# Kernel tuning notes

Hardware: AMD Instinct MI355X
Metric: run time of the kernel (lower is better)

The kernel has to match this reference:

```python
import jax, jax.numpy as jnp
import numpy as np

N_NODES = 50000
N_EDGES = 800000
NUM_FEATS = 128
HIDDEN = 256
NUM_GRAPHS = 512
BN_EPS = 1e-5


def setup_inputs() -> dict:
    key = jax.random.key(0)
    ks = jax.random.split(key, 12)
    x = jax.random.normal(ks[0], (N_NODES, NUM_FEATS), dtype=jnp.float32)
    edge_index = jax.random.randint(ks[1], (2, N_EDGES), 0, N_NODES, dtype=jnp.int64)
    batch = jnp.sort(jax.random.randint(ks[2], (N_NODES,), 0, NUM_GRAPHS, dtype=jnp.int64))
    s1 = 1.0 / np.sqrt(NUM_FEATS)
    s2 = 1.0 / np.sqrt(HIDDEN)
    return {
        "x": x,
        "edge_index": edge_index,
        "batch": batch,
        "w1a": jax.random.normal(ks[3], (NUM_FEATS, HIDDEN), dtype=jnp.float32) * s1,
        "b1a": jnp.zeros((HIDDEN,), jnp.float32),
        "w2a": jax.random.normal(ks[4], (HIDDEN, HIDDEN), dtype=jnp.float32) * s2,
        "b2a": jnp.zeros((HIDDEN,), jnp.float32),
        "ga": jnp.ones((HIDDEN,), jnp.float32),
        "ba": jnp.zeros((HIDDEN,), jnp.float32),
        "w1s": jax.random.normal(ks[5], (2, HIDDEN, HIDDEN), dtype=jnp.float32) * s2,
        "b1s": jnp.zeros((2, HIDDEN), jnp.float32),
        "w2s": jax.random.normal(ks[6], (2, HIDDEN, HIDDEN), dtype=jnp.float32) * s2,
        "b2s": jnp.zeros((2, HIDDEN), jnp.float32),
        "gs": jnp.ones((2, HIDDEN), jnp.float32),
        "bs": jnp.zeros((2, HIDDEN), jnp.float32),
    }


def _gin_layer(h, src, dst, w1, b1, w2, b2, gamma, beta):
    # GIN aggregation: (1 + eps=0) * x + sum over in-neighbors
    agg = jax.ops.segment_sum(h[src], dst, num_segments=N_NODES)
    z = h + agg
    z = jax.nn.relu(z @ w1 + b1)
    z = jax.nn.relu(z @ w2 + b2)
    # BatchNorm1d (training mode: biased batch statistics over nodes)
    mu = jnp.mean(z, axis=0)
    var = jnp.var(z, axis=0)
    return gamma * (z - mu) * jax.lax.rsqrt(var + BN_EPS) + beta


def reference(x, edge_index, batch, w1a, b1a, w2a, b2a, ga, ba,
              w1s, b1s, w2s, b2s, gs, bs):
    src, dst = edge_index[0], edge_index[1]
    h = _gin_layer(x, src, dst, w1a, b1a, w2a, b2a, ga, ba)
    for i in range(w1s.shape[0]):
        h = _gin_layer(h, src, dst, w1s[i], b1s[i], w2s[i], b2s[i], gs[i], bs[i])
    # global_mean_pool over graph ids
    sums = jax.ops.segment_sum(h, batch, num_segments=NUM_GRAPHS)
    counts = jax.ops.segment_sum(jnp.ones((h.shape[0],), h.dtype), batch,
                                 num_segments=NUM_GRAPHS)
    return sums / jnp.maximum(counts, 1.0)[:, None]
```

## Files before the change

kernel.cpp:

```cpp
#include <hip/hip_runtime.h>
#include <cstdint>
#include <cstddef>


constexpr int N_NODES  = 50000;
constexpr int N_EDGES  = 800000;
constexpr int F_IN     = 128;
constexpr int HID      = 256;
constexpr int N_GRAPHS = 512;
constexpr float BN_EPS = 1e-5f;

constexpr int SCAN_CHUNK = 4096;
constexpr int SCAN_NB    = (N_NODES + SCAN_CHUNK - 1) / SCAN_CHUNK;

typedef unsigned short u16;
typedef u16 u16x2 __attribute__((ext_vector_type(2)));
typedef u16 u16x4 __attribute__((ext_vector_type(4)));
typedef u16 u16x8 __attribute__((ext_vector_type(8)));
typedef __bf16 bf16x8 __attribute__((ext_vector_type(8)));
typedef float f32x4 __attribute__((ext_vector_type(4)));

__device__ __forceinline__ u16 f2bf(float f) {
    uint32_t u = __float_as_uint(f);
    uint32_t r = (u + 0x7FFFu + ((u >> 16) & 1u)) >> 16;
    return (u16)r;
}
__device__ __forceinline__ float bf2f(u16 h) {
    return __uint_as_float(((uint32_t)h) << 16);
}

__device__ __forceinline__ void gload16(const void* g, void* l) {
    __builtin_amdgcn_global_load_lds(
        (const __attribute__((address_space(1))) uint32_t*)g,
        (__attribute__((address_space(3))) uint32_t*)l, 16, 0, 0);
}

__global__ void f2bf_k(const float* __restrict__ in, u16* __restrict__ outp, int n8) {
    int i = blockIdx.x * 256 + threadIdx.x;
    if (i >= n8) return;
    float4 a = reinterpret_cast<const float4*>(in)[i * 2];
    float4 b = reinterpret_cast<const float4*>(in)[i * 2 + 1];
    u16x8 v;
    v[0] = f2bf(a.x); v[1] = f2bf(a.y); v[2] = f2bf(a.z); v[3] = f2bf(a.w);
    v[4] = f2bf(b.x); v[5] = f2bf(b.y); v[6] = f2bf(b.z); v[7] = f2bf(b.w);
    reinterpret_cast<u16x8*>(outp)[i] = v;
}

__global__ void hist_k(const int* __restrict__ dst, int* __restrict__ deg) {
    int e = blockIdx.x * 256 + threadIdx.x;
    if (e < N_EDGES) atomicAdd(&deg[dst[e]], 1);
}

__global__ void scan_part1(const int* __restrict__ in, int* __restrict__ bsum) {
    __shared__ int sm[256];
    int t = threadIdx.x;
    int base = blockIdx.x * SCAN_CHUNK + t * 16;
    int s = 0;
#pragma unroll
    for (int j = 0; j < 16; j++) { int idx = base + j; s += (idx < N_NODES) ? in[idx] : 0; }
    sm[t] = s; __syncthreads();
    for (int off = 128; off > 0; off >>= 1) {
        if (t < off) sm[t] += sm[t + off];
        __syncthreads();
    }
    if (t == 0) bsum[blockIdx.x] = sm[0];
}

__global__ void scan_tops(int* __restrict__ bsum, int* __restrict__ rowptr) {
    if (threadIdx.x == 0 && blockIdx.x == 0) {
        int acc = 0;
        for (int i = 0; i < SCAN_NB; i++) { int v = bsum[i]; bsum[i] = acc; acc += v; }
        rowptr[N_NODES] = acc;
    }
}

__global__ void scan_final(const int* __restrict__ in, const int* __restrict__ bsum,
                           int* __restrict__ rowptr, int* __restrict__ cursor) {
    __shared__ int sm[256];
    int t = threadIdx.x;
    int base = blockIdx.x * SCAN_CHUNK + t * 16;
    int loc[16]; int s = 0;
#pragma unroll
    for (int j = 0; j < 16; j++) { int idx = base + j; loc[j] = s; s += (idx < N_NODES) ? in[idx] : 0; }
    sm[t] = s; __syncthreads();
    for (int off = 1; off < 256; off <<= 1) {
        int v = (t >= off) ? sm[t - off] : 0;
        __syncthreads();
        sm[t] += v;
        __syncthreads();
    }
    int excl = sm[t] - s + bsum[blockIdx.x];
#pragma unroll
    for (int j = 0; j < 16; j++) {
        int idx = base + j;
        if (idx < N_NODES) { int rp = excl + loc[j]; rowptr[idx] = rp; cursor[idx] = rp; }
    }
}

__global__ void build_csr(const int* __restrict__ src, const int* __restrict__ dst,
                          int* __restrict__ cursor, int* __restrict__ col) {
    int e = blockIdx.x * 256 + threadIdx.x;
    if (e < N_EDGES) {
        int d = dst[e];
        int p = atomicAdd(&cursor[d], 1);
        col[p] = src[e];
    }
}

template <int F, bool FOLD>
__global__ __launch_bounds__(256) void aggregate_k(const u16* __restrict__ h,
                                                   const int* __restrict__ rowptr,
                                                   const int* __restrict__ col,
                                                   const float* __restrict__ stats,
                                                   const float* __restrict__ gamma,
                                                   const float* __restrict__ beta,
                                                   u16* __restrict__ outp) {
    int node = blockIdx.x * 4 + (threadIdx.x >> 6);
    if (node >= N_NODES) return;
    int lane = threadIdx.x & 63;
    int beg = rowptr[node], end = rowptr[node + 1];
    if constexpr (F == 256) {
        float sc[4], sh[4];
        if constexpr (FOLD) {
            int c4 = lane * 4;
#pragma unroll
            for (int i = 0; i < 4; i++) {
                float mu  = stats[c4 + i] * (1.f / N_NODES);
                float var = stats[HID + c4 + i] * (1.f / N_NODES) - mu * mu;
                float g = gamma[c4 + i] * rsqrtf(var + BN_EPS);
                sc[i] = g;
                sh[i] = beta[c4 + i] - mu * g;
            }
        }
        const u16x4* hp = reinterpret_cast<const u16x4*>(h);
        u16x4 sv = hp[(size_t)node * 64 + lane];
        float acc[4] = {bf2f(sv[0]), bf2f(sv[1]), bf2f(sv[2]), bf2f(sv[3])};
        int e = beg;
        for (; e + 4 <= end; e += 4) {
            int s0 = col[e], s1 = col[e + 1], s2 = col[e + 2], s3 = col[e + 3];
            u16x4 v0 = hp[(size_t)s0 * 64 + lane];
            u16x4 v1 = hp[(size_t)s1 * 64 + lane];
            u16x4 v2 = hp[(size_t)s2 * 64 + lane];
            u16x4 v3 = hp[(size_t)s3 * 64 + lane];
#pragma unroll
            for (int i = 0; i < 4; i++)
                acc[i] += (bf2f(v0[i]) + bf2f(v1[i])) + (bf2f(v2[i]) + bf2f(v3[i]));
        }
        for (; e < end; ++e) {
            int s = col[e];
            u16x4 v = hp[(size_t)s * 64 + lane];
#pragma unroll
            for (int i = 0; i < 4; i++) acc[i] += bf2f(v[i]);
        }
        if constexpr (FOLD) {
            float m = (float)(end - beg + 1);
#pragma unroll
            for (int i = 0; i < 4; i++) acc[i] = acc[i] * sc[i] + m * sh[i];
        }
        u16x4 r;
#pragma unroll
        for (int i = 0; i < 4; i++) r[i] = f2bf(acc[i]);
        reinterpret_cast<u16x4*>(outp)[(size_t)node * 64 + lane] = r;
    } else {
        const u16x2* hp = reinterpret_cast<const u16x2*>(h);
        u16x2 sv = hp[(size_t)node * 64 + lane];
        float acc[2] = {bf2f(sv[0]), bf2f(sv[1])};
        int e = beg;
        for (; e + 4 <= end; e += 4) {
            int s0 = col[e], s1 = col[e + 1], s2 = col[e + 2], s3 = col[e + 3];
            u16x2 v0 = hp[(size_t)s0 * 64 + lane];
            u16x2 v1 = hp[(size_t)s1 * 64 + lane];
            u16x2 v2 = hp[(size_t)s2 * 64 + lane];
            u16x2 v3 = hp[(size_t)s3 * 64 + lane];
#pragma unroll
            for (int i = 0; i < 2; i++)
                acc[i] += (bf2f(v0[i]) + bf2f(v1[i])) + (bf2f(v2[i]) + bf2f(v3[i]));
        }
        for (; e < end; ++e) {
            int s = col[e];
            u16x2 v = hp[(size_t)s * 64 + lane];
#pragma unroll
            for (int i = 0; i < 2; i++) acc[i] += bf2f(v[i]);
        }
        u16x2 r;
        r[0] = f2bf(acc[0]); r[1] = f2bf(acc[1]);
        reinterpret_cast<u16x2*>(outp)[(size_t)node * 64 + lane] = r;
    }
}

__global__ void wsplit_all(const float* __restrict__ w1a, const float* __restrict__ w2a,
                           const float* __restrict__ w1s, const float* __restrict__ w2s,
                           u16* __restrict__ th, u16* __restrict__ tl) {
    int idx = blockIdx.x * 256 + threadIdx.x;
    const float* W; int local; size_t dof;
    if (idx < 32768)       { W = w1a;         local = idx;          dof = 0; }
    else if (idx < 98304)  { W = w2a;         local = idx - 32768;  dof = 32768; }
    else if (idx < 163840) { W = w1s;         local = idx - 98304;  dof = 98304; }
    else if (idx < 229376) { W = w1s + 65536; local = idx - 163840; dof = 163840; }
    else if (idx < 294912) { W = w2s;         local = idx - 229376; dof = 229376; }
    else if (idx < 360448) { W = w2s + 65536; local = idx - 294912; dof = 294912; }
    else return;
    int n = local & 255, k = local >> 8;
    float f = W[(size_t)k * 256 + n];
    u16 h = f2bf(f);
    int t = k >> 5, j = (k >> 3) & 3, e = k & 7;
    int uo = j ^ ((n >> 1) & 3);
    size_t di = dof + (size_t)t * 8192 + n * 32 + uo * 8 + e;
    th[di] = h;
    tl[di] = f2bf(f - bf2f(h));
}

template <int K, bool STATS>
__global__ __launch_bounds__(256, 2) void gemm_mfma(const u16* __restrict__ A,
                                                    const u16* __restrict__ Wth,
                                                    const u16* __restrict__ Wtl,
                                                    const float* __restrict__ bias,
                                                    u16* __restrict__ C,
                                                    float* __restrict__ stats) {
    constexpr int BM = 128, BK = 32;
    __shared__ alignas(16) u16 Ah[BM * BK];
    __shared__ alignas(16) u16 Bh[HID * BK];
    __shared__ alignas(16) u16 Bl[HID * BK];
    __shared__ float smsum[HID];
    __shared__ float smsq[HID];

    const int tid  = threadIdx.x;
    const int r0   = blockIdx.x * BM;
    const int lane = tid & 63, wv = tid >> 6;
    const int wm = wv >> 1, wn = wv & 1;
    const int l15 = lane & 15, kg = lane >> 4;

    int aro[2], aco[2];
#pragma unroll
    for (int p = 0; p < 2; p++) {
        int nu = wv * 128 + p * 64 + lane;
        int r = nu >> 2, us = nu & 3;
        int u = us ^ ((r >> 1) & 3);
        aro[p] = r;
        aco[p] = u * 8;
    }

    f32x4 acc[4][8];
#pragma unroll
    for (int i = 0; i < 4; i++)
#pragma unroll
        for (int j = 0; j < 8; j++) acc[i][j] = (f32x4){0.f, 0.f, 0.f, 0.f};

    for (int k0 = 0; k0 < K; k0 += BK) {
        int t = k0 >> 5;
#pragma unroll
        for (int p = 0; p < 2; p++) {
            const u16* src = A + (size_t)(r0 + aro[p]) * K + k0 + aco[p];
            gload16(src, (char*)Ah + (size_t)(wv * 2 + p) * 1024);
        }
        const char* wh = (const char*)Wth + (size_t)t * 16384 + (size_t)wv * 4096 + (size_t)lane * 16;
        const char* wl = (const char*)Wtl + (size_t)t * 16384 + (size_t)wv * 4096 + (size_t)lane * 16;
#pragma unroll
        for (int c = 0; c < 4; c++) {
            gload16(wh + c * 1024, (char*)Bh + (size_t)wv * 4096 + c * 1024);
            gload16(wl + c * 1024, (char*)Bl + (size_t)wv * 4096 + c * 1024);
        }
        __syncthreads();
        bf16x8 ah[4];
#pragma unroll
        for (int mi = 0; mi < 4; mi++) {
            int r = wm * 64 + mi * 16 + l15;
            int off = r * 64 + ((kg ^ ((r >> 1) & 3)) << 4);
            ah[mi] = __builtin_bit_cast(bf16x8, *reinterpret_cast<const u16x8*>((const char*)Ah + off));
        }
#pragma unroll
        for (int ni = 0; ni < 8; ni++) {
            int n = wn * 128 + ni * 16 + l15;
            int off = n * 64 + ((kg ^ ((n >> 1) & 3)) << 4);
            bf16x8 bh = __builtin_bit_cast(bf16x8, *reinterpret_cast<const u16x8*>((const char*)Bh + off));
            bf16x8 bl = __builtin_bit_cast(bf16x8, *reinterpret_cast<const u16x8*>((const char*)Bl + off));
#pragma unroll
            for (int mi = 0; mi < 4; mi++) {
                acc[mi][ni] = __builtin_amdgcn_mfma_f32_16x16x32_bf16(ah[mi], bh, acc[mi][ni], 0, 0, 0);
                acc[mi][ni] = __builtin_amdgcn_mfma_f32_16x16x32_bf16(ah[mi], bl, acc[mi][ni], 0, 0, 0);
            }
        }
        __syncthreads();
    }
    if constexpr (STATS) {
        smsum[tid] = 0.f;
        smsq[tid]  = 0.f;
        __syncthreads();
    }
    float bv[8];
#pragma unroll
    for (int ni = 0; ni < 8; ni++) bv[ni] = bias[wn * 128 + ni * 16 + l15];
    float ps[8] = {}, pq[8] = {};
#pragma unroll
    for (int mi = 0; mi < 4; mi++) {
        int rowb = r0 + wm * 64 + mi * 16 + kg * 4;
#pragma unroll
        for (int rr = 0; rr < 4; rr++) {
            int row = rowb + rr;
            if (row < N_NODES) {
                u16* cp = C + (size_t)row * HID + wn * 128 + l15;
#pragma unroll
                for (int ni = 0; ni < 8; ni++) {
                    float v = fmaxf(acc[mi][ni][rr] + bv[ni], 0.f);
                    cp[ni * 16] = f2bf(v);
                    if constexpr (STATS) { ps[ni] += v; pq[ni] += v * v; }
                }
            }
        }
    }
    if constexpr (STATS) {
#pragma unroll
        for (int ni = 0; ni < 8; ni++) {
            int c = wn * 128 + ni * 16 + l15;
            atomicAdd(&smsum[c], ps[ni]);
            atomicAdd(&smsq[c], pq[ni]);
        }
        __syncthreads();
        atomicAdd(&stats[tid], smsum[tid]);
        atomicAdd(&stats[HID + tid], smsq[tid]);
    }
}

__device__ __forceinline__ int lowerb(const int* a, int key) {
    int lo = 0, hi = N_NODES;
    while (lo < hi) { int mid = (lo + hi) >> 1; if (a[mid] < key) lo = mid + 1; else hi = mid; }
    return lo;
}

__global__ void pool_k(const u16* __restrict__ h, const int* __restrict__ batch,
                       const float* __restrict__ stats, const float* __restrict__ gamma,
                       const float* __restrict__ beta, float* __restrict__ out) {
    __shared__ int bnd[2];
    int g = blockIdx.x;
    if (threadIdx.x == 0) bnd[0] = lowerb(batch, g);
    if (threadIdx.x == 1) bnd[1] = lowerb(batch, g + 1);
    __syncthreads();
    int lo = bnd[0], hi = bnd[1];
    int c = threadIdx.x;
    float mu  = stats[c] * (1.f / N_NODES);
    float var = stats[HID + c] * (1.f / N_NODES) - mu * mu;
    float sc = gamma[c] * rsqrtf(var + BN_EPS);
    float sh = beta[c] - mu * sc;
    float s = 0.f;
    for (int r = lo; r < hi; ++r) s += bf2f(h[(size_t)r * HID + c]);
    int cnt = hi - lo;
    float v = (cnt > 0) ? (sc * (s / (float)cnt) + sh) : 0.f;
    out[(size_t)g * HID + c] = v;
}

extern "C" void kernel_launch(void* const* d_in, const int* in_sizes, int n_in,
                              void* d_out, int out_size, void* d_ws, size_t ws_size,
                              hipStream_t stream) {
    const float* x   = (const float*)d_in[0];
    const int*   ei  = (const int*)d_in[1];
    const int* batch = (const int*)d_in[2];
    const float* w1a = (const float*)d_in[3];
    const float* b1a = (const float*)d_in[4];
    const float* w2a = (const float*)d_in[5];
    const float* b2a = (const float*)d_in[6];
    const float* ga  = (const float*)d_in[7];
    const float* ba  = (const float*)d_in[8];
    const float* w1s = (const float*)d_in[9];
    const float* b1s = (const float*)d_in[10];
    const float* w2s = (const float*)d_in[11];
    const float* b2s = (const float*)d_in[12];
    const float* gs  = (const float*)d_in[13];
    const float* bs  = (const float*)d_in[14];
    const int* src = ei;
    const int* dst = ei + N_EDGES;

    char* ws = (char*)d_ws;
    size_t off = 0;
    auto alloc = [&](size_t bytes) { void* p = ws + off; off += (bytes + 255) & ~(size_t)255; return p; };
    u16* A      = (u16*)alloc(sizeof(u16) * (size_t)N_NODES * HID);
    u16* B      = (u16*)alloc(sizeof(u16) * (size_t)N_NODES * HID);
    u16* Xb     = (u16*)alloc(sizeof(u16) * (size_t)N_NODES * F_IN);
    int* rowptr = (int*)alloc(sizeof(int) * (N_NODES + 1));
    int* deg    = (int*)alloc(sizeof(int) * N_NODES);
    int* cursor = (int*)alloc(sizeof(int) * N_NODES);
    int* col    = (int*)alloc(sizeof(int) * N_EDGES);
    int* bsum   = (int*)alloc(sizeof(int) * 64);
    float* stats  = (float*)alloc(sizeof(float) * 512 * 3);
    constexpr size_t WT_TOT = 32768 + 5 * 65536;
    u16* WtH = (u16*)alloc(sizeof(u16) * WT_TOT);
    u16* WtL = (u16*)alloc(sizeof(u16) * WT_TOT);
    constexpr size_t o1a = 0, o2a = 32768, o1s0 = 98304, o1s1 = 163840, o2s0 = 229376, o2s1 = 294912;
    float* out    = (float*)d_out;
    (void)ws_size; (void)in_sizes; (void)n_in; (void)out_size;

    f2bf_k<<<(N_NODES * F_IN / 8 + 255) / 256, 256, 0, stream>>>(x, Xb, N_NODES * F_IN / 8);
    wsplit_all<<<(360448 + 255) / 256, 256, 0, stream>>>(w1a, w2a, w1s, w2s, WtH, WtL);
    hipMemsetAsync(stats, 0, sizeof(float) * 512 * 3, stream);

    hipMemsetAsync(deg, 0, sizeof(int) * N_NODES, stream);
    hist_k<<<N_EDGES / 256, 256, 0, stream>>>(dst, deg);
    scan_part1<<<SCAN_NB, 256, 0, stream>>>(deg, bsum);
    scan_tops<<<1, 64, 0, stream>>>(bsum, rowptr);
    scan_final<<<SCAN_NB, 256, 0, stream>>>(deg, bsum, rowptr, cursor);
    build_csr<<<N_EDGES / 256, 256, 0, stream>>>(src, dst, cursor, col);

    const int AGG_GRID  = (N_NODES + 3) / 4;
    const int GEMM_GRID = (N_NODES + 127) / 128;

    aggregate_k<128, false><<<AGG_GRID, 256, 0, stream>>>(Xb, rowptr, col, nullptr, nullptr, nullptr, A);
    gemm_mfma<128, false><<<GEMM_GRID, 256, 0, stream>>>(A, WtH + o1a, WtL + o1a, b1a, B, nullptr);
    gemm_mfma<256, true><<<GEMM_GRID, 256, 0, stream>>>(B, WtH + o2a, WtL + o2a, b2a, B, stats);

    aggregate_k<256, true><<<AGG_GRID, 256, 0, stream>>>(B, rowptr, col, stats, ga, ba, A);
    gemm_mfma<256, false><<<GEMM_GRID, 256, 0, stream>>>(A, WtH + o1s0, WtL + o1s0, b1s, A, nullptr);
    gemm_mfma<256, true><<<GEMM_GRID, 256, 0, stream>>>(A, WtH + o2s0, WtL + o2s0, b2s, A, stats + 512);

    aggregate_k<256, true><<<AGG_GRID, 256, 0, stream>>>(A, rowptr, col, stats + 512, gs, bs, B);
    gemm_mfma<256, false><<<GEMM_GRID, 256, 0, stream>>>(B, WtH + o1s1, WtL + o1s1, b1s + 256, B, nullptr);
    gemm_mfma<256, true><<<GEMM_GRID, 256, 0, stream>>>(B, WtH + o2s1, WtL + o2s1, b2s + 256, B, stats + 1024);

    pool_k<<<N_GRAPHS, 256, 0, stream>>>(B, batch, stats + 1024, gs + 256, bs + 256, out);
}
```

Baseline: 461.0 us.

## Slice features into column panels and aggregate per-XCC slice with work-stealing

Stores hidden activations in feature-sliced panels (32 bf16 columns per slice, 16 fp32 for the input) so each gather pass touches a compact slice that can stay resident in one XCC's L2. Aggregation kernels read the hardware XCC id and start on a 'home' slice, then use atomic chunk counters to steal work across all eight slices. GEMMs gain templated addressing for sliced inputs and outputs. Input x stays fp32 in the sliced layout instead of being converted to bf16 first. This trades fully coalesced row access, one bf16 conversion pass and simple launches for better gather cache locality. It adds atomic and barrier overhead and scattered narrow GEMM stores.

```diff
diff --git a/kernel.cpp b/kernel.cpp
--- a/kernel.cpp
+++ b/kernel.cpp
@@ -12,6 +12,7 @@
 
 constexpr int SCAN_CHUNK = 4096;
 constexpr int SCAN_NB    = (N_NODES + SCAN_CHUNK - 1) / SCAN_CHUNK;
+constexpr int NCHUNK     = (N_NODES + 63) / 64;
 
 typedef unsigned short u16;
 typedef u16 u16x2 __attribute__((ext_vector_type(2)));
@@ -29,21 +30,26 @@
     return __uint_as_float(((uint32_t)h) << 16);
 }
 
+__device__ __forceinline__ int xcc_id() {
+    int x;
+    asm volatile("s_getreg_b32 %0, hwreg(HW_REG_XCC_ID)" : "=s"(x));
+    return x & 7;
+}
+
 __device__ __forceinline__ void gload16(const void* g, void* l) {
     __builtin_amdgcn_global_load_lds(
         (const __attribute__((address_space(1))) uint32_t*)g,
         (__attribute__((address_space(3))) uint32_t*)l, 16, 0, 0);
 }
 
-__global__ void f2bf_k(const float* __restrict__ in, u16* __restrict__ outp, int n8) {
+__global__ void reslice_x(const float* __restrict__ x, float* __restrict__ xs) {
     int i = blockIdx.x * 256 + threadIdx.x;
-    if (i >= n8) return;
-    float4 a = reinterpret_cast<const float4*>(in)[i * 2];
-    float4 b = reinterpret_cast<const float4*>(in)[i * 2 + 1];
-    u16x8 v;
-    v[0] = f2bf(a.x); v[1] = f2bf(a.y); v[2] = f2bf(a.z); v[3] = f2bf(a.w);
-    v[4] = f2bf(b.x); v[5] = f2bf(b.y); v[6] = f2bf(b.z); v[7] = f2bf(b.w);
-    reinterpret_cast<u16x8*>(outp)[i] = v;
+    if (i >= N_NODES * 32) return;
+    int n = i >> 5, u = i & 31;
+    int f = u * 4;
+    int sl = f >> 4, w = f & 15;
+    float4 v = reinterpret_cast<const float4*>(x)[i];
+    *reinterpret_cast<float4*>(&xs[(size_t)sl * N_NODES * 16 + (size_t)n * 16 + w]) = v;
 }
 
 __global__ void hist_k(const int* __restrict__ dst, int* __restrict__ deg) {
@@ -107,84 +113,127 @@
     }
 }
 
-template <int F, bool FOLD>
-__global__ __launch_bounds__(256) void aggregate_k(const u16* __restrict__ h,
-                                                   const int* __restrict__ rowptr,
-                                                   const int* __restrict__ col,
-                                                   const float* __restrict__ stats,
-                                                   const float* __restrict__ gamma,
-                                                   const float* __restrict__ beta,
-                                                   u16* __restrict__ outp) {
-    int node = blockIdx.x * 4 + (threadIdx.x >> 6);
-    if (node >= N_NODES) return;
-    int lane = threadIdx.x & 63;
-    int beg = rowptr[node], end = rowptr[node + 1];
-    if constexpr (F == 256) {
+__global__ __launch_bounds__(256) void agg_x(const float* __restrict__ xs,
+                                             const int* __restrict__ rowptr,
+                                             const int* __restrict__ col,
+                                             int* __restrict__ cur,
+                                             u16* __restrict__ outp) {
+    __shared__ int smc;
+    const int tid = threadIdx.x;
+    const int g = tid >> 3, l = tid & 7;
+    const int home = xcc_id();
+    for (int pass = 0; pass < 8; ++pass) {
+        int s = (home + pass) & 7;
+        const float2* xp = reinterpret_cast<const float2*>(xs + (size_t)s * N_NODES * 16);
+        u16x2* op = reinterpret_cast<u16x2*>(outp + (size_t)s * N_NODES * 16);
+        while (true) {
+            __syncthreads();
+            if (tid == 0) smc = atomicAdd(&cur[s], 1);
+            __syncthreads();
+            int chunk = smc;
+            if (chunk >= NCHUNK) break;
+#pragma unroll
+            for (int half = 0; half < 2; ++half) {
+                int n = chunk * 64 + half * 32 + g;
+                if (n >= N_NODES) continue;
+                int beg = rowptr[n], end = rowptr[n + 1];
+                float2 a = xp[(size_t)n * 8 + l];
+                int e = beg;
+                for (; e + 4 <= end; e += 4) {
+                    int s0 = __builtin_nontemporal_load(col + e);
+                    int s1 = __builtin_nontemporal_load(col + e + 1);
+                    int s2 = __builtin_nontemporal_load(col + e + 2);
+                    int s3 = __builtin_nontemporal_load(col + e + 3);
+                    float2 v0 = xp[(size_t)s0 * 8 + l];
+                    float2 v1 = xp[(size_t)s1 * 8 + l];
+                    float2 v2 = xp[(size_t)s2 * 8 + l];
+                    float2 v3 = xp[(size_t)s3 * 8 + l];
+                    a.x += (v0.x + v1.x) + (v2.x + v3.x);
+                    a.y += (v0.y + v1.y) + (v2.y + v3.y);
+                }
+                for (; e < end; ++e) {
+                    float2 v = xp[(size_t)__builtin_nontemporal_load(col + e) * 8 + l];
+                    a.x += v.x; a.y += v.y;
+                }
+                u16x2 r; r[0] = f2bf(a.x); r[1] = f2bf(a.y);
+                __builtin_nontemporal_store(r, &op[(size_t)n * 8 + l]);
+            }
+        }
+    }
+}
+
+template <bool FOLD>
+__global__ __launch_bounds__(256) void agg_h(const u16* __restrict__ h,
+                                             const int* __restrict__ rowptr,
+                                             const int* __restrict__ col,
+                                             const float* __restrict__ stats,
+                                             const float* __restrict__ gamma,
+                                             const float* __restrict__ beta,
+                                             int* __restrict__ cur,
+                                             u16* __restrict__ outp) {
+    __shared__ int smc;
+    const int tid = threadIdx.x;
+    const int g = tid >> 3, l = tid & 7;
+    const int home = xcc_id();
+    for (int pass = 0; pass < 8; ++pass) {
+        int s = (home + pass) & 7;
+        const u16x4* hp = reinterpret_cast<const u16x4*>(h + (size_t)s * N_NODES * 32);
+        u16x4* op = reinterpret_cast<u16x4*>(outp + (size_t)s * N_NODES * 32);
         float sc[4], sh[4];
         if constexpr (FOLD) {
-            int c4 = lane * 4;
+            int c4 = s * 32 + l * 4;
 #pragma unroll
             for (int i = 0; i < 4; i++) {
                 float mu  = stats[c4 + i] * (1.f / N_NODES);
                 float var = stats[HID + c4 + i] * (1.f / N_NODES) - mu * mu;
-                float g = gamma[c4 + i] * rsqrtf(var + BN_EPS);
-                sc[i] = g;
-                sh[i] = beta[c4 + i] - mu * g;
-            }
-        }
-        const u16x4* hp = reinterpret_cast<const u16x4*>(h);
-        u16x4 sv = hp[(size_t)node * 64 + lane];
-        float acc[4] = {bf2f(sv[0]), bf2f(sv[1]), bf2f(sv[2]), bf2f(sv[3])};
-        int e = beg;
-        for (; e + 4 <= end; e += 4) {
-            int s0 = col[e], s1 = col[e + 1], s2 = col[e + 2], s3 = col[e + 3];
-            u16x4 v0 = hp[(size_t)s0 * 64 + lane];
-            u16x4 v1 = hp[(size_t)s1 * 64 + lane];
-            u16x4 v2 = hp[(size_t)s2 * 64 + lane];
-            u16x4 v3 = hp[(size_t)s3 * 64 + lane];
-#pragma unroll
-            for (int i = 0; i < 4; i++)
-                acc[i] += (bf2f(v0[i]) + bf2f(v1[i])) + (bf2f(v2[i]) + bf2f(v3[i]));
-        }
-        for (; e < end; ++e) {
-            int s = col[e];
-            u16x4 v = hp[(size_t)s * 64 + lane];
-#pragma unroll
-            for (int i = 0; i < 4; i++) acc[i] += bf2f(v[i]);
-        }
-        if constexpr (FOLD) {
-            float m = (float)(end - beg + 1);
-#pragma unroll
-            for (int i = 0; i < 4; i++) acc[i] = acc[i] * sc[i] + m * sh[i];
-        }
-        u16x4 r;
-#pragma unroll
-        for (int i = 0; i < 4; i++) r[i] = f2bf(acc[i]);
-        reinterpret_cast<u16x4*>(outp)[(size_t)node * 64 + lane] = r;
-    } else {
-        const u16x2* hp = reinterpret_cast<const u16x2*>(h);
-        u16x2 sv = hp[(size_t)node * 64 + lane];
-        float acc[2] = {bf2f(sv[0]), bf2f(sv[1])};
-        int e = beg;
-        for (; e + 4 <= end; e += 4) {
-            int s0 = col[e], s1 = col[e + 1], s2 = col[e + 2], s3 = col[e + 3];
-            u16x2 v0 = hp[(size_t)s0 * 64 + lane];
-            u16x2 v1 = hp[(size_t)s1 * 64 + lane];
-            u16x2 v2 = hp[(size_t)s2 * 64 + lane];
-            u16x2 v3 = hp[(size_t)s3 * 64 + lane];
-#pragma unroll
-            for (int i = 0; i < 2; i++)
-                acc[i] += (bf2f(v0[i]) + bf2f(v1[i])) + (bf2f(v2[i]) + bf2f(v3[i]));
-        }
-        for (; e < end; ++e) {
-            int s = col[e];
-            u16x2 v = hp[(size_t)s * 64 + lane];
-#pragma unroll
-            for (int i = 0; i < 2; i++) acc[i] += bf2f(v[i]);
-        }
-        u16x2 r;
-        r[0] = f2bf(acc[0]); r[1] = f2bf(acc[1]);
-        reinterpret_cast<u16x2*>(outp)[(size_t)node * 64 + lane] = r;
+                float gg = gamma[c4 + i] * rsqrtf(var + BN_EPS);
+                sc[i] = gg;
+                sh[i] = beta[c4 + i] - mu * gg;
+            }
+        }
+        while (true) {
+            __syncthreads();
+            if (tid == 0) smc = atomicAdd(&cur[s], 1);
+            __syncthreads();
+            int chunk = smc;
+            if (chunk >= NCHUNK) break;
+#pragma unroll
+            for (int half = 0; half < 2; ++half) {
+                int n = chunk * 64 + half * 32 + g;
+                if (n >= N_NODES) continue;
+                int beg = rowptr[n], end = rowptr[n + 1];
+                u16x4 sv = hp[(size_t)n * 8 + l];
+                float a[4] = {bf2f(sv[0]), bf2f(sv[1]), bf2f(sv[2]), bf2f(sv[3])};
+                int e = beg;
+                for (; e + 4 <= end; e += 4) {
+                    int s0 = __builtin_nontemporal_load(col + e);
+                    int s1 = __builtin_nontemporal_load(col + e + 1);
+                    int s2 = __builtin_nontemporal_load(col + e + 2);
+                    int s3 = __builtin_nontemporal_load(col + e + 3);
+                    u16x4 v0 = hp[(size_t)s0 * 8 + l];
+                    u16x4 v1 = hp[(size_t)s1 * 8 + l];
+                    u16x4 v2 = hp[(size_t)s2 * 8 + l];
+                    u16x4 v3 = hp[(size_t)s3 * 8 + l];
+#pragma unroll
+                    for (int i = 0; i < 4; i++)
+                        a[i] += (bf2f(v0[i]) + bf2f(v1[i])) + (bf2f(v2[i]) + bf2f(v3[i]));
+                }
+                for (; e < end; ++e) {
+                    u16x4 v = hp[(size_t)__builtin_nontemporal_load(col + e) * 8 + l];
+#pragma unroll
+                    for (int i = 0; i < 4; i++) a[i] += bf2f(v[i]);
+                }
+                if constexpr (FOLD) {
+                    float m = (float)(end - beg + 1);
+#pragma unroll
+                    for (int i = 0; i < 4; i++) a[i] = a[i] * sc[i] + m * sh[i];
+                }
+                u16x4 r;
+#pragma unroll
+                for (int i = 0; i < 4; i++) r[i] = f2bf(a[i]);
+                __builtin_nontemporal_store(r, &op[(size_t)n * 8 + l]);
+            }
+        }
     }
 }
 
@@ -210,7 +259,7 @@
     tl[di] = f2bf(f - bf2f(h));
 }
 
-template <int K, bool STATS>
+template <int K, bool STATS, int ASL, bool CSL>
 __global__ __launch_bounds__(256, 2) void gemm_mfma(const u16* __restrict__ A,
                                                     const u16* __restrict__ Wth,
                                                     const u16* __restrict__ Wtl,
@@ -250,7 +299,15 @@
         int t = k0 >> 5;
 #pragma unroll
         for (int p = 0; p < 2; p++) {
-            const u16* src = A + (size_t)(r0 + aro[p]) * K + k0 + aco[p];
+            const u16* src;
+            if constexpr (ASL == 0) {
+                src = A + (size_t)(r0 + aro[p]) * K + k0 + aco[p];
+            } else if constexpr (ASL == 1) {
+                src = A + (size_t)t * (N_NODES * 32) + (size_t)(r0 + aro[p]) * 32 + aco[p];
+            } else {
+                int f = k0 + aco[p];
+                src = A + (size_t)(f >> 4) * (N_NODES * 16) + (size_t)(r0 + aro[p]) * 16 + (f & 15);
+            }
             gload16(src, (char*)Ah + (size_t)(wv * 2 + p) * 1024);
         }
         const char* wh = (const char*)Wth + (size_t)t * 16384 + (size_t)wv * 4096 + (size_t)lane * 16;
@@ -298,11 +355,15 @@
         for (int rr = 0; rr < 4; rr++) {
             int row = rowb + rr;
             if (row < N_NODES) {
-                u16* cp = C + (size_t)row * HID + wn * 128 + l15;
 #pragma unroll
                 for (int ni = 0; ni < 8; ni++) {
                     float v = fmaxf(acc[mi][ni][rr] + bv[ni], 0.f);
-                    cp[ni * 16] = f2bf(v);
+                    int c = wn * 128 + ni * 16 + l15;
+                    if constexpr (CSL) {
+                        C[(size_t)(c >> 5) * (N_NODES * 32) + (size_t)row * 32 + (c & 31)] = f2bf(v);
+                    } else {
+                        C[(size_t)row * HID + c] = f2bf(v);
+                    }
                     if constexpr (STATS) { ps[ni] += v; pq[ni] += v * v; }
                 }
             }
@@ -341,8 +402,9 @@
     float var = stats[HID + c] * (1.f / N_NODES) - mu * mu;
     float sc = gamma[c] * rsqrtf(var + BN_EPS);
     float sh = beta[c] - mu * sc;
+    const u16* hc = h + (size_t)(c >> 5) * (N_NODES * 32) + (c & 31);
     float s = 0.f;
-    for (int r = lo; r < hi; ++r) s += bf2f(h[(size_t)r * HID + c]);
+    for (int r = lo; r < hi; ++r) s += bf2f(hc[(size_t)r * 32]);
     int cnt = hi - lo;
     float v = (cnt > 0) ? (sc * (s / (float)cnt) + sh) : 0.f;
     out[(size_t)g * HID + c] = v;
@@ -372,15 +434,18 @@
     char* ws = (char*)d_ws;
     size_t off = 0;
     auto alloc = [&](size_t bytes) { void* p = ws + off; off += (bytes + 255) & ~(size_t)255; return p; };
-    u16* A      = (u16*)alloc(sizeof(u16) * (size_t)N_NODES * HID);
-    u16* B      = (u16*)alloc(sizeof(u16) * (size_t)N_NODES * HID);
-    u16* Xb     = (u16*)alloc(sizeof(u16) * (size_t)N_NODES * F_IN);
+    u16* P      = (u16*)alloc(sizeof(u16) * (size_t)N_NODES * HID);
+    u16* Q      = (u16*)alloc(sizeof(u16) * (size_t)N_NODES * HID);
+    u16* Z      = (u16*)alloc(sizeof(u16) * (size_t)N_NODES * HID);
+    float* Xs   = (float*)Z;
+    static_assert(sizeof(u16) * (size_t)N_NODES * HID == sizeof(float) * (size_t)N_NODES * F_IN, "alias");
     int* rowptr = (int*)alloc(sizeof(int) * (N_NODES + 1));
     int* deg    = (int*)alloc(sizeof(int) * N_NODES);
     int* cursor = (int*)alloc(sizeof(int) * N_NODES);
     int* col    = (int*)alloc(sizeof(int) * N_EDGES);
     int* bsum   = (int*)alloc(sizeof(int) * 64);
     float* stats  = (float*)alloc(sizeof(float) * 512 * 3);
+    int* cur    = (int*)alloc(sizeof(int) * 24);
     constexpr size_t WT_TOT = 32768 + 5 * 65536;
     u16* WtH = (u16*)alloc(sizeof(u16) * WT_TOT);
     u16* WtL = (u16*)alloc(sizeof(u16) * WT_TOT);
@@ -388,9 +453,10 @@
     float* out    = (float*)d_out;
     (void)ws_size; (void)in_sizes; (void)n_in; (void)out_size;
 
-    f2bf_k<<<(N_NODES * F_IN / 8 + 255) / 256, 256, 0, stream>>>(x, Xb, N_NODES * F_IN / 8);
+    reslice_x<<<(N_NODES * 32 + 255) / 256, 256, 0, stream>>>(x, Xs);
     wsplit_all<<<(360448 + 255) / 256, 256, 0, stream>>>(w1a, w2a, w1s, w2s, WtH, WtL);
     hipMemsetAsync(stats, 0, sizeof(float) * 512 * 3, stream);
+    hipMemsetAsync(cur, 0, sizeof(int) * 24, stream);
 
     hipMemsetAsync(deg, 0, sizeof(int) * N_NODES, stream);
     hist_k<<<N_EDGES / 256, 256, 0, stream>>>(dst, deg);
@@ -399,20 +465,20 @@
     scan_final<<<SCAN_NB, 256, 0, stream>>>(deg, bsum, rowptr, cursor);
     build_csr<<<N_EDGES / 256, 256, 0, stream>>>(src, dst, cursor, col);
 
-    const int AGG_GRID  = (N_NODES + 3) / 4;
+    const int AGG_GRID  = 1024;
     const int GEMM_GRID = (N_NODES + 127) / 128;
 
-    aggregate_k<128, false><<<AGG_GRID, 256, 0, stream>>>(Xb, rowptr, col, nullptr, nullptr, nullptr, A);
-    gemm_mfma<128, false><<<GEMM_GRID, 256, 0, stream>>>(A, WtH + o1a, WtL + o1a, b1a, B, nullptr);
-    gemm_mfma<256, true><<<GEMM_GRID, 256, 0, stream>>>(B, WtH + o2a, WtL + o2a, b2a, B, stats);
-
-    aggregate_k<256, true><<<AGG_GRID, 256, 0, stream>>>(B, rowptr, col, stats, ga, ba, A);
-    gemm_mfma<256, false><<<GEMM_GRID, 256, 0, stream>>>(A, WtH + o1s0, WtL + o1s0, b1s, A, nullptr);
-    gemm_mfma<256, true><<<GEMM_GRID, 256, 0, stream>>>(A, WtH + o2s0, WtL + o2s0, b2s, A, stats + 512);
-
-    aggregate_k<256, true><<<AGG_GRID, 256, 0, stream>>>(A, rowptr, col, stats + 512, gs, bs, B);
-    gemm_mfma<256, false><<<GEMM_GRID, 256, 0, stream>>>(B, WtH + o1s1, WtL + o1s1, b1s + 256, B, nullptr);
-    gemm_mfma<256, true><<<GEMM_GRID, 256, 0, stream>>>(B, WtH + o2s1, WtL + o2s1, b2s + 256, B, stats + 1024);
-
-    pool_k<<<N_GRAPHS, 256, 0, stream>>>(B, batch, stats + 1024, gs + 256, bs + 256, out);
-}
+    agg_x<<<AGG_GRID, 256, 0, stream>>>(Xs, rowptr, col, cur, P);
+    gemm_mfma<128, false, 2, false><<<GEMM_GRID, 256, 0, stream>>>(P, WtH + o1a, WtL + o1a, b1a, Z, nullptr);
+    gemm_mfma<256, true, 0, true><<<GEMM_GRID, 256, 0, stream>>>(Z, WtH + o2a, WtL + o2a, b2a, Q, stats);
+
+    agg_h<true><<<AGG_GRID, 256, 0, stream>>>(Q, rowptr, col, stats, ga, ba, cur + 8, P);
+    gemm_mfma<256, false, 1, false><<<GEMM_GRID, 256, 0, stream>>>(P, WtH + o1s0, WtL + o1s0, b1s, Z, nullptr);
+    gemm_mfma<256, true, 0, true><<<GEMM_GRID, 256, 0, stream>>>(Z, WtH + o2s0, WtL + o2s0, b2s, Q, stats + 512);
+
+    agg_h<true><<<AGG_GRID, 256, 0, stream>>>(Q, rowptr, col, stats + 512, gs, bs, cur + 16, P);
+    gemm_mfma<256, false, 1, false><<<GEMM_GRID, 256, 0, stream>>>(P, WtH + o1s1, WtL + o1s1, b1s + 256, Z, nullptr);
+    gemm_mfma<256, true, 0, true><<<GEMM_GRID, 256, 0, stream>>>(Z, WtH + o2s1, WtL + o2s1, b2s + 256, Q, stats + 1024);
+
+    pool_k<<<N_GRAPHS, 256, 0, stream>>>(Q, batch, stats + 1024, gs + 256, bs + 256, out);
+}
```

Result: slower. 900.3 us (+95.3%).

## Fuse both MLP GEMMs per GIN layer into one kernel with LDS-resident intermediate

Applied to the files above, without the earlier changes.

Replaces the two back-to-back GEMM launches per layer with one kernel. It computes the first GEMM plus ReLU into a 64x256 bf16 tile held in shared memory, then runs the second GEMM directly from that tile, followed by the bias, ReLU, output store and BatchNorm statistics. This removes the global write and re-read of the hidden activation and one launch per layer. In exchange the row tile shrinks from 128 to 64 rows, so weight tiles are re-fetched by twice as many blocks. Shared memory use also rises to about 66KB per block, which may limit occupancy.

```diff
diff --git a/kernel.cpp b/kernel.cpp
--- a/kernel.cpp
+++ b/kernel.cpp
@@ -210,51 +210,50 @@
     tl[di] = f2bf(f - bf2f(h));
 }
 
-template <int K, bool STATS>
-__global__ __launch_bounds__(256, 2) void gemm_mfma(const u16* __restrict__ A,
-                                                    const u16* __restrict__ Wth,
-                                                    const u16* __restrict__ Wtl,
-                                                    const float* __restrict__ bias,
-                                                    u16* __restrict__ C,
-                                                    float* __restrict__ stats) {
-    constexpr int BM = 128, BK = 32;
-    __shared__ alignas(16) u16 Ah[BM * BK];
+template <int K1>
+__global__ __launch_bounds__(256, 2) void mlp_k(const u16* __restrict__ A,
+                                                const u16* __restrict__ W1h,
+                                                const u16* __restrict__ W1l,
+                                                const float* __restrict__ b1,
+                                                const u16* __restrict__ W2h,
+                                                const u16* __restrict__ W2l,
+                                                const float* __restrict__ b2,
+                                                u16* __restrict__ C,
+                                                float* __restrict__ stats) {
+    constexpr int BM = 64, BK = 32;
+    __shared__ alignas(16) u16 Z1[BM * HID];
     __shared__ alignas(16) u16 Bh[HID * BK];
     __shared__ alignas(16) u16 Bl[HID * BK];
     __shared__ float smsum[HID];
     __shared__ float smsq[HID];
+    u16* Ah = Z1;
 
     const int tid  = threadIdx.x;
     const int r0   = blockIdx.x * BM;
     const int lane = tid & 63, wv = tid >> 6;
-    const int wm = wv >> 1, wn = wv & 1;
+    const int wn = wv;
     const int l15 = lane & 15, kg = lane >> 4;
 
-    int aro[2], aco[2];
-#pragma unroll
-    for (int p = 0; p < 2; p++) {
-        int nu = wv * 128 + p * 64 + lane;
+    int aro, aco;
+    {
+        int nu = wv * 64 + lane;
         int r = nu >> 2, us = nu & 3;
         int u = us ^ ((r >> 1) & 3);
-        aro[p] = r;
-        aco[p] = u * 8;
-    }
-
-    f32x4 acc[4][8];
+        aro = r;
+        aco = u * 8;
+    }
+
+    f32x4 acc[4][4];
 #pragma unroll
     for (int i = 0; i < 4; i++)
 #pragma unroll
-        for (int j = 0; j < 8; j++) acc[i][j] = (f32x4){0.f, 0.f, 0.f, 0.f};
-
-    for (int k0 = 0; k0 < K; k0 += BK) {
+        for (int j = 0; j < 4; j++) acc[i][j] = (f32x4){0.f, 0.f, 0.f, 0.f};
+
+    for (int k0 = 0; k0 < K1; k0 += BK) {
         int t = k0 >> 5;
-#pragma unroll
-        for (int p = 0; p < 2; p++) {
-            const u16* src = A + (size_t)(r0 + aro[p]) * K + k0 + aco[p];
-            gload16(src, (char*)Ah + (size_t)(wv * 2 + p) * 1024);
-        }
-        const char* wh = (const char*)Wth + (size_t)t * 16384 + (size_t)wv * 4096 + (size_t)lane * 16;
-        const char* wl = (const char*)Wtl + (size_t)t * 16384 + (size_t)wv * 4096 + (size_t)lane * 16;
+        gload16(A + (size_t)(r0 + aro) * K1 + k0 + aco, (char*)Ah + (size_t)wv * 1024);
+        const char* wh = (const char*)W1h + (size_t)t * 16384 + (size_t)wv * 4096 + (size_t)lane * 16;
+        const char* wl = (const char*)W1l + (size_t)t * 16384 + (size_t)wv * 4096 + (size_t)lane * 16;
 #pragma unroll
         for (int c = 0; c < 4; c++) {
             gload16(wh + c * 1024, (char*)Bh + (size_t)wv * 4096 + c * 1024);
@@ -264,13 +263,13 @@
         bf16x8 ah[4];
 #pragma unroll
         for (int mi = 0; mi < 4; mi++) {
-            int r = wm * 64 + mi * 16 + l15;
+            int r = mi * 16 + l15;
             int off = r * 64 + ((kg ^ ((r >> 1) & 3)) << 4);
             ah[mi] = __builtin_bit_cast(bf16x8, *reinterpret_cast<const u16x8*>((const char*)Ah + off));
         }
 #pragma unroll
-        for (int ni = 0; ni < 8; ni++) {
-            int n = wn * 128 + ni * 16 + l15;
+        for (int ni = 0; ni < 4; ni++) {
+            int n = wn * 64 + ni * 16 + l15;
             int off = n * 64 + ((kg ^ ((n >> 1) & 3)) << 4);
             bf16x8 bh = __builtin_bit_cast(bf16x8, *reinterpret_cast<const u16x8*>((const char*)Bh + off));
             bf16x8 bl = __builtin_bit_cast(bf16x8, *reinterpret_cast<const u16x8*>((const char*)Bl + off));
@@ -282,43 +281,98 @@
         }
         __syncthreads();
     }
-    if constexpr (STATS) {
-        smsum[tid] = 0.f;
-        smsq[tid]  = 0.f;
-        __syncthreads();
-    }
-    float bv[8];
-#pragma unroll
-    for (int ni = 0; ni < 8; ni++) bv[ni] = bias[wn * 128 + ni * 16 + l15];
-    float ps[8] = {}, pq[8] = {};
+    {
+        float bv[4];
+#pragma unroll
+        for (int ni = 0; ni < 4; ni++) bv[ni] = b1[wn * 64 + ni * 16 + l15];
+#pragma unroll
+        for (int mi = 0; mi < 4; mi++) {
+#pragma unroll
+            for (int rr = 0; rr < 4; rr++) {
+                int r = mi * 16 + kg * 4 + rr;
+#pragma unroll
+                for (int ni = 0; ni < 4; ni++) {
+                    float v = fmaxf(acc[mi][ni][rr] + bv[ni], 0.f);
+                    int c = wn * 64 + ni * 16 + l15;
+                    int us = (c >> 3) ^ (r & 7);
+                    reinterpret_cast<u16*>((char*)Z1 + r * 512 + us * 16)[c & 7] = f2bf(v);
+                }
+            }
+        }
+        __syncthreads();
+    }
+
+#pragma unroll
+    for (int i = 0; i < 4; i++)
+#pragma unroll
+        for (int j = 0; j < 4; j++) acc[i][j] = (f32x4){0.f, 0.f, 0.f, 0.f};
+    for (int k0 = 0; k0 < HID; k0 += BK) {
+        int t = k0 >> 5;
+        const char* wh = (const char*)W2h + (size_t)t * 16384 + (size_t)wv * 4096 + (size_t)lane * 16;
+        const char* wl = (const char*)W2l + (size_t)t * 16384 + (size_t)wv * 4096 + (size_t)lane * 16;
+#pragma unroll
+        for (int c = 0; c < 4; c++) {
+            gload16(wh + c * 1024, (char*)Bh + (size_t)wv * 4096 + c * 1024);
+            gload16(wl + c * 1024, (char*)Bl + (size_t)wv * 4096 + c * 1024);
+        }
+        __syncthreads();
+        bf16x8 ah[4];
+#pragma unroll
+        for (int mi = 0; mi < 4; mi++) {
+            int r = mi * 16 + l15;
+            int u = (k0 >> 3) + kg;
+            int us = u ^ (r & 7);
+            ah[mi] = __builtin_bit_cast(bf16x8,
+                *reinterpret_cast<const u16x8*>((const char*)Z1 + r * 512 + us * 16));
+        }
+#pragma unroll
+        for (int ni = 0; ni < 4; ni++) {
+            int n = wn * 64 + ni * 16 + l15;
+            int off = n * 64 + ((kg ^ ((n >> 1) & 3)) << 4);
+            bf16x8 bh = __builtin_bit_cast(bf16x8, *reinterpret_cast<const u16x8*>((const char*)Bh + off));
+            bf16x8 bl = __builtin_bit_cast(bf16x8, *reinterpret_cast<const u16x8*>((const char*)Bl + off));
+#pragma unroll
+            for (int mi = 0; mi < 4; mi++) {
+                acc[mi][ni] = __builtin_amdgcn_mfma_f32_16x16x32_bf16(ah[mi], bh, acc[mi][ni], 0, 0, 0);
+                acc[mi][ni] = __builtin_amdgcn_mfma_f32_16x16x32_bf16(ah[mi], bl, acc[mi][ni], 0, 0, 0);
+            }
+        }
+        __syncthreads();
+    }
+
+    smsum[tid] = 0.f;
+    smsq[tid]  = 0.f;
+    __syncthreads();
+    float bv[4];
+#pragma unroll
+    for (int ni = 0; ni < 4; ni++) bv[ni] = b2[wn * 64 + ni * 16 + l15];
+    float ps[4] = {}, pq[4] = {};
 #pragma unroll
     for (int mi = 0; mi < 4; mi++) {
-        int rowb = r0 + wm * 64 + mi * 16 + kg * 4;
+        int rowb = r0 + mi * 16 + kg * 4;
 #pragma unroll
         for (int rr = 0; rr < 4; rr++) {
             int row = rowb + rr;
             if (row < N_NODES) {
-                u16* cp = C + (size_t)row * HID + wn * 128 + l15;
-#pragma unroll
-                for (int ni = 0; ni < 8; ni++) {
+                u16* cp = C + (size_t)row * HID + wn * 64 + l15;
+#pragma unroll
+                for (int ni = 0; ni < 4; ni++) {
                     float v = fmaxf(acc[mi][ni][rr] + bv[ni], 0.f);
                     cp[ni * 16] = f2bf(v);
-                    if constexpr (STATS) { ps[ni] += v; pq[ni] += v * v; }
+                    ps[ni] += v; pq[ni] += v * v;
                 }
             }
         }
     }
-    if constexpr (STATS) {
-#pragma unroll
-        for (int ni = 0; ni < 8; ni++) {
-            int c = wn * 128 + ni * 16 + l15;
-            atomicAdd(&smsum[c], ps[ni]);
-            atomicAdd(&smsq[c], pq[ni]);
-        }
-        __syncthreads();
-        atomicAdd(&stats[tid], smsum[tid]);
-        atomicAdd(&stats[HID + tid], smsq[tid]);
-    }
+#pragma unroll
+    for (int ni = 0; ni < 4; ni++) {
+        int c = wn * 64 + ni * 16 + l15;
+        atomicAdd(&smsum[c], ps[ni]);
+        atomicAdd(&smsq[c], pq[ni]);
+    }
+    __syncthreads();
+    atomicAdd(&stats[tid], smsum[tid]);
+    atomicAdd(&stats[HID + tid], smsq[tid]);
 }
 
 __device__ __forceinline__ int lowerb(const int* a, int key) {
@@ -399,20 +453,20 @@
     scan_final<<<SCAN_NB, 256, 0, stream>>>(deg, bsum, rowptr, cursor);
     build_csr<<<N_EDGES / 256, 256, 0, stream>>>(src, dst, cursor, col);
 
-    const int AGG_GRID  = (N_NODES + 3) / 4;
-    const int GEMM_GRID = (N_NODES + 127) / 128;
+    const int AGG_GRID = (N_NODES + 3) / 4;
+    const int MLP_GRID = (N_NODES + 63) / 64;
 
     aggregate_k<128, false><<<AGG_GRID, 256, 0, stream>>>(Xb, rowptr, col, nullptr, nullptr, nullptr, A);
-    gemm_mfma<128, false><<<GEMM_GRID, 256, 0, stream>>>(A, WtH + o1a, WtL + o1a, b1a, B, nullptr);
-    gemm_mfma<256, true><<<GEMM_GRID, 256, 0, stream>>>(B, WtH + o2a, WtL + o2a, b2a, B, stats);
+    mlp_k<128><<<MLP_GRID, 256, 0, stream>>>(A, WtH + o1a, WtL + o1a, b1a,
+                                             WtH + o2a, WtL + o2a, b2a, B, stats);
 
     aggregate_k<256, true><<<AGG_GRID, 256, 0, stream>>>(B, rowptr, col, stats, ga, ba, A);
-    gemm_mfma<256, false><<<GEMM_GRID, 256, 0, stream>>>(A, WtH + o1s0, WtL + o1s0, b1s, A, nullptr);
-    gemm_mfma<256, true><<<GEMM_GRID, 256, 0, stream>>>(A, WtH + o2s0, WtL + o2s0, b2s, A, stats + 512);
+    mlp_k<256><<<MLP_GRID, 256, 0, stream>>>(A, WtH + o1s0, WtL + o1s0, b1s,
+                                             WtH + o2s0, WtL + o2s0, b2s, A, stats + 512);
 
     aggregate_k<256, true><<<AGG_GRID, 256, 0, stream>>>(A, rowptr, col, stats + 512, gs, bs, B);
-    gemm_mfma<256, false><<<GEMM_GRID, 256, 0, stream>>>(B, WtH + o1s1, WtL + o1s1, b1s + 256, B, nullptr);
-    gemm_mfma<256, true><<<GEMM_GRID, 256, 0, stream>>>(B, WtH + o2s1, WtL + o2s1, b2s + 256, B, stats + 1024);
+    mlp_k<256><<<MLP_GRID, 256, 0, stream>>>(B, WtH + o1s1, WtL + o1s1, b1s + 256,
+                                             WtH + o2s1, WtL + o2s1, b2s + 256, B, stats + 1024);
 
     pool_k<<<N_GRAPHS, 256, 0, stream>>>(B, batch, stats + 1024, gs + 256, bs + 256, out);
 }
```

Measured after the change: 483.5 us. 1.05x slower.
